# Performance work log

Measured on AMD Instinct MI355X. Metric: run time of the kernel, lower is better.

The kernel has to match this reference:

```python
import jax, jax.numpy as jnp
import numpy as np


def setup_inputs() -> dict:
    key = jax.random.key(0)
    k1, k2, k3 = jax.random.split(key, 3)
    B, S_TOT, HD = 2, 4096, 1024
    return {
        "q": jax.random.normal(k1, (B, S_TOT, HD), dtype=jnp.float32),
        "k": jax.random.normal(k2, (B, S_TOT, HD), dtype=jnp.float32),
        "v": jax.random.normal(k3, (B, S_TOT, HD), dtype=jnp.float32),
        "num_heads": 16,
        "num_shots": 4,
        "per_g": 64,
    }


def reference(q, k, v, num_heads, num_shots, per_g):
    # Equal-length shots: shot_latent_indices = [0, L, 2L, ..., s_tot] per batch.
    b, s_tot, hd = q.shape
    d = hd // num_heads
    L = s_tot // num_shots  # local shot length
    scale = 1.0 / jnp.sqrt(jnp.asarray(d, q.dtype))

    # [b, S, L, H, D]
    qs = q.reshape(b, num_shots, L, num_heads, d)
    ks = k.reshape(b, num_shots, L, num_heads, d)
    vs = v.reshape(b, num_shots, L, num_heads, d)

    # Global pool: first per_g tokens of each shot ('firstk'), shared by all shots.
    kg = ks[:, :, :per_g].reshape(b, num_shots * per_g, num_heads, d)  # [b, G, H, D]
    vg = vs[:, :, :per_g].reshape(b, num_shots * per_g, num_heads, d)

    # Block-local scores [b,S,H,L,L] and shared-global scores [b,S,H,L,G]
    s_loc = jnp.einsum("bsqhd,bskhd->bshqk", qs, ks) * scale
    s_glb = jnp.einsum("bsqhd,bghd->bshqg", qs, kg) * scale
    logits = jnp.concatenate([s_loc, s_glb], axis=-1)  # [b,S,H,L,L+G]
    p = jax.nn.softmax(logits, axis=-1)

    o_loc = jnp.einsum("bshqk,bskhd->bsqhd", p[..., :L], vs)
    o_glb = jnp.einsum("bshqg,bghd->bsqhd", p[..., L:], vg)
    out = (o_loc + o_glb).reshape(b, s_tot, hd)
    return out
```

## Files before the change

### kernel.cpp

```cpp
#include <hip/hip_runtime.h>
#include <hip/hip_bf16.h>

#define S_TOT 4096
#define HDIM  1024
#define NH    16
#define DH    64
#define L_    1024
#define NT    19

using bf16x8 = __attribute__((ext_vector_type(8))) short;
using f32x16 = __attribute__((ext_vector_type(16))) float;
using i32x4  = __attribute__((ext_vector_type(4))) int;

typedef const __attribute__((address_space(1))) unsigned int* gp1_t;
typedef __attribute__((address_space(3))) unsigned int* lp3_t;

__device__ __forceinline__ short f2bf(float f) {
    union { float f; unsigned u; } x; x.f = f;
    unsigned r = x.u + 0x7FFFu + ((x.u >> 16) & 1u);
    return (short)(r >> 16);
}

__device__ __forceinline__ unsigned cvt_pk_bf16(float lo, float hi) {
    unsigned r;
    asm("v_cvt_pk_bf16_f32 %0, %1, %2" : "=v"(r) : "v"(lo), "v"(hi));
    return r;
}

__device__ __forceinline__ float exp2_fast(float x) {
#if __has_builtin(__builtin_amdgcn_exp2f)
    return __builtin_amdgcn_exp2f(x);
#else
    return exp2f(x);
#endif
}

__device__ __forceinline__ void gload16(const void* g, void* l) {
    __builtin_amdgcn_global_load_lds((gp1_t)g, (lp3_t)(unsigned long)(l), 16, 0, 0);
}

__global__ __launch_bounds__(256) void prep_kv(
    const float* __restrict__ kf, const float* __restrict__ vf,
    short* __restrict__ kb, short* __restrict__ vb)
{
    __shared__ short st[64 * 70];
    const int bid = blockIdx.x, tid = threadIdx.x;
    if (bid < 1024) {
        const int gid = bid * 256 + tid;
        #pragma unroll
        for (int it = 0; it < 2; ++it) {
            size_t e = ((size_t)gid + (size_t)it * 262144) * 16;
            #pragma unroll
            for (int half = 0; half < 2; ++half) {
                float4 a = *(const float4*)(kf + e + half * 8);
                float4 c = *(const float4*)(kf + e + half * 8 + 4);
                bf16x8 r;
                r[0]=f2bf(a.x); r[1]=f2bf(a.y); r[2]=f2bf(a.z); r[3]=f2bf(a.w);
                r[4]=f2bf(c.x); r[5]=f2bf(c.y); r[6]=f2bf(c.z); r[7]=f2bf(c.w);
                *(bf16x8*)(kb + e + half * 8) = r;
            }
        }
    } else {
        const int vbid = bid - 1024;
        const int stile = vbid & 63, ht = (vbid >> 6) & 15, b = vbid >> 10;
        const int rt = tid >> 2, q4 = tid & 3;
        const float* src = vf + ((size_t)(b * S_TOT + stile * 64 + rt)) * HDIM + ht * 64 + q4 * 16;
        short* dst = st + rt * 70 + q4 * 16;
        #pragma unroll
        for (int i = 0; i < 4; ++i) {
            float4 x = *(const float4*)(src + i * 4);
            dst[i*4+0] = f2bf(x.x); dst[i*4+1] = f2bf(x.y);
            dst[i*4+2] = f2bf(x.z); dst[i*4+3] = f2bf(x.w);
        }
        __syncthreads();
        const int orow = tid >> 2, oq = tid & 3;
        bf16x8 o0, o1;
        #pragma unroll
        for (int j = 0; j < 8; ++j) o0[j] = st[(oq * 16 + j) * 70 + orow];
        #pragma unroll
        for (int j = 0; j < 8; ++j) o1[j] = st[(oq * 16 + 8 + j) * 70 + orow];
        short* dst2 = vb + ((size_t)((b * NH + ht) * 64 + orow)) * S_TOT + stile * 64 + oq * 16;
        *(bf16x8*)dst2 = o0;
        *(bf16x8*)(dst2 + 8) = o1;
    }
}

__global__ __launch_bounds__(128, 2) void attn_kernel(
    const float* __restrict__ qf, const short* __restrict__ kb,
    const short* __restrict__ vb, float* __restrict__ out)
{
    __shared__ __align__(16) char smem[32768];
    const int tid  = threadIdx.x;
    const int wave = tid >> 6, lane = tid & 63;
    const int hi   = lane >> 5, q32 = lane & 31;

    const int bidhw = blockIdx.x;
    const int bid = ((bidhw & 7) << 7) | (bidhw >> 3);
    const int qt = bid & 7, h = (bid >> 3) & 15, s = (bid >> 7) & 3, b = bid >> 9;

    const float CSC = 0.125f * 1.4426950408889634f;
    bf16x8 qv[2][4];
    #pragma unroll
    for (int qs = 0; qs < 2; ++qs) {
        const float* qp = qf + ((size_t)(b*S_TOT + s*L_ + qt*128 + wave*64 + qs*32 + q32)) * HDIM
                             + h * DH + hi * 8;
        #pragma unroll
        for (int d = 0; d < 4; ++d) {
            float4 x0 = *(const float4*)(qp + d * 16);
            float4 x1 = *(const float4*)(qp + d * 16 + 4);
            i32x4 u;
            u[0] = (int)cvt_pk_bf16(x0.x * CSC, x0.y * CSC);
            u[1] = (int)cvt_pk_bf16(x0.z * CSC, x0.w * CSC);
            u[2] = (int)cvt_pk_bf16(x1.x * CSC, x1.y * CSC);
            u[3] = (int)cvt_pk_bf16(x1.z * CSC, x1.w * CSC);
            qv[qs][d] = __builtin_bit_cast(bf16x8, u);
        }
    }

    const int r_low = (wave << 3) | (lane >> 3);
    const int lch   = (lane & 7) ^ (lane >> 3);
    const int krow_low = (r_low & 3) | ((r_low & 4) << 1) | ((r_low & 8) >> 1);
    const size_t ko = (size_t)krow_low * 2048 + (lch << 4);
    const size_t vo = (size_t)r_low * 8192 + (lch << 4);
    const char* kbase = (const char*)kb + ((size_t)b * S_TOT) * 2048 + h * 128;
    const char* vbase = (const char*)vb + ((size_t)(b * NH + h)) * (64ull * 8192);

    auto abs_tile_of = [&](int t) -> int {
        if (t < 16) return s * 16 + t;
        int g = t - 16; if (g >= s) ++g;
        return g * 16;
    };
    auto stage = [&](int t, int bo) {
        const int at = abs_tile_of(t);
        const char* kp = kbase + (size_t)at * 131072;
        const char* vp = vbase + (size_t)at * 128;
        char* dK = smem + bo + wave * 1024;
        char* dV = dK + 8192;
        #pragma unroll
        for (int i = 0; i < 4; ++i)
            gload16(kp + ko + (size_t)i * 32768, dK + i * 2048);
        #pragma unroll
        for (int i = 0; i < 4; ++i)
            gload16(vp + vo + (size_t)i * 131072, dV + i * 2048);
    };

    int qc[4];
    #pragma unroll
    for (int i = 0; i < 4; ++i)
        qc[i] = q32 * 128 + (((i * 2 + hi) ^ (q32 & 7)) << 4);

    f32x16 zro;
    #pragma unroll
    for (int r = 0; r < 16; ++r) zro[r] = 0.f;
    f32x16 acc[2][2];
    acc[0][0] = zro; acc[0][1] = zro; acc[1][0] = zro; acc[1][1] = zro;
    float ps[2] = {0.f, 0.f};

    #define CHUNK(RB, HF, BIAS) do {                                               \
        f32x16 S_[2];                                                              \
        {                                                                          \
            __builtin_amdgcn_s_setprio(1);                                         \
            bf16x8 f0 = *(const bf16x8*)(smem + (RB) + (HF)*4096 + qc[0]);         \
            bf16x8 f1 = *(const bf16x8*)(smem + (RB) + (HF)*4096 + qc[1]);         \
            bf16x8 f2 = *(const bf16x8*)(smem + (RB) + (HF)*4096 + qc[2]);         \
            bf16x8 f3 = *(const bf16x8*)(smem + (RB) + (HF)*4096 + qc[3]);         \
            _Pragma("unroll")                                                      \
            for (int qs = 0; qs < 2; ++qs) {                                       \
                f32x16 a = __builtin_amdgcn_mfma_f32_32x32x16_bf16(f0, qv[qs][0], zro, 0,0,0); \
                a = __builtin_amdgcn_mfma_f32_32x32x16_bf16(f1, qv[qs][1], a, 0,0,0); \
                a = __builtin_amdgcn_mfma_f32_32x32x16_bf16(f2, qv[qs][2], a, 0,0,0); \
                a = __builtin_amdgcn_mfma_f32_32x32x16_bf16(f3, qv[qs][3], a, 0,0,0); \
                S_[qs] = a;                                                        \
            }                                                                      \
            __builtin_amdgcn_s_setprio(0);                                         \
        }                                                                          \
        _Pragma("unroll")                                                          \
        for (int qs = 0; qs < 2; ++qs) {                                           \
            _Pragma("unroll")                                                      \
            for (int r = 0; r < 16; ++r)                                           \
                S_[qs][r] = exp2_fast(S_[qs][r] + (BIAS));                         \
            float s0 = (S_[qs][0] + S_[qs][1]) + (S_[qs][2] + S_[qs][3]);          \
            float s1 = (S_[qs][4] + S_[qs][5]) + (S_[qs][6] + S_[qs][7]);          \
            float s2 = (S_[qs][8] + S_[qs][9]) + (S_[qs][10] + S_[qs][11]);        \
            float s3 = (S_[qs][12] + S_[qs][13]) + (S_[qs][14] + S_[qs][15]);      \
            ps[qs] += (s0 + s1) + (s2 + s3);                                       \
        }                                                                          \
        bf16x8 pf0_[2], pf1_[2];                                                   \
        _Pragma("unroll")                                                          \
        for (int qs = 0; qs < 2; ++qs) {                                           \
            i32x4 u;                                                               \
            u[0] = (int)cvt_pk_bf16(S_[qs][0],  S_[qs][1]);                        \
            u[1] = (int)cvt_pk_bf16(S_[qs][2],  S_[qs][3]);                        \
            u[2] = (int)cvt_pk_bf16(S_[qs][4],  S_[qs][5]);                        \
            u[3] = (int)cvt_pk_bf16(S_[qs][6],  S_[qs][7]);                        \
            pf0_[qs] = __builtin_bit_cast(bf16x8, u);                              \
            u[0] = (int)cvt_pk_bf16(S_[qs][8],  S_[qs][9]);                        \
            u[1] = (int)cvt_pk_bf16(S_[qs][10], S_[qs][11]);                       \
            u[2] = (int)cvt_pk_bf16(S_[qs][12], S_[qs][13]);                       \
            u[3] = (int)cvt_pk_bf16(S_[qs][14], S_[qs][15]);                       \
            pf1_[qs] = __builtin_bit_cast(bf16x8, u);                              \
        }                                                                          \
        {                                                                          \
            __builtin_amdgcn_s_setprio(1);                                         \
            bf16x8 w00 = *(const bf16x8*)(smem + (RB) + 8192  + qc[2*(HF)]);       \
            bf16x8 w01 = *(const bf16x8*)(smem + (RB) + 8192  + qc[2*(HF)+1]);     \
            bf16x8 w10 = *(const bf16x8*)(smem + (RB) + 12288 + qc[2*(HF)]);       \
            bf16x8 w11 = *(const bf16x8*)(smem + (RB) + 12288 + qc[2*(HF)+1]);     \
            _Pragma("unroll")                                                      \
            for (int qs = 0; qs < 2; ++qs) {                                       \
                acc[qs][0] = __builtin_amdgcn_mfma_f32_32x32x16_bf16(w00, pf0_[qs], acc[qs][0], 0,0,0); \
                acc[qs][0] = __builtin_amdgcn_mfma_f32_32x32x16_bf16(w01, pf1_[qs], acc[qs][0], 0,0,0); \
                acc[qs][1] = __builtin_amdgcn_mfma_f32_32x32x16_bf16(w10, pf0_[qs], acc[qs][1], 0,0,0); \
                acc[qs][1] = __builtin_amdgcn_mfma_f32_32x32x16_bf16(w11, pf1_[qs], acc[qs][1], 0,0,0); \
            }                                                                      \
            __builtin_amdgcn_s_setprio(0);                                         \
        }                                                                          \
    } while (0)

    #define BARRIER() do {                                                         \
        __builtin_amdgcn_sched_barrier(0);                                         \
        __builtin_amdgcn_s_barrier();                                              \
        __builtin_amdgcn_sched_barrier(0);                                         \
    } while (0)

    stage(0, 0);
    asm volatile("s_waitcnt vmcnt(0)" ::: "memory");
    BARRIER();

    int bufo = 0;
    for (int t = 0; t < NT; ++t) {
        if (t + 1 < NT) {
            stage(t + 1, bufo ^ 16384);
            asm volatile("s_waitcnt vmcnt(8)" ::: "memory");
        } else {
            asm volatile("s_waitcnt vmcnt(0)" ::: "memory");
        }
        BARRIER();
        const float bias = (t == 0) ? 1.0f : 0.0f;
        CHUNK(bufo, 0, bias);
        CHUNK(bufo, 1, bias);
        BARRIER();
        bufo ^= 16384;
    }

    #pragma unroll
    for (int qs = 0; qs < 2; ++qs) {
        float tot = ps[qs] + __shfl_xor(ps[qs], 32);
        float inv = 1.0f / tot;
        const size_t orow = (size_t)(b*S_TOT + s*L_ + qt*128 + wave*64 + qs*32 + q32);
        float* op = out + orow * HDIM + h * DH;
        #pragma unroll
        for (int m = 0; m < 4; ++m) {
            float4 w0, w1;
            w0.x = acc[qs][0][4*m+0]*inv; w0.y = acc[qs][0][4*m+1]*inv;
            w0.z = acc[qs][0][4*m+2]*inv; w0.w = acc[qs][0][4*m+3]*inv;
            *(float4*)(op + 8*m + 4*hi) = w0;
            w1.x = acc[qs][1][4*m+0]*inv; w1.y = acc[qs][1][4*m+1]*inv;
            w1.z = acc[qs][1][4*m+2]*inv; w1.w = acc[qs][1][4*m+3]*inv;
            *(float4*)(op + 32 + 8*m + 4*hi) = w1;
        }
    }
}

extern "C" void kernel_launch(void* const* d_in, const int* in_sizes, int n_in,
                              void* d_out, int out_size, void* d_ws, size_t ws_size,
                              hipStream_t stream) {
    const float* q = (const float*)d_in[0];
    const float* k = (const float*)d_in[1];
    const float* v = (const float*)d_in[2];
    char* ws = (char*)d_ws;
    short* kbuf = (short*)(ws);
    short* vbuf = (short*)(ws + (16u << 20));
    prep_kv<<<dim3(3072), dim3(256), 0, stream>>>(k, v, kbuf, vbuf);
    attn_kernel<<<dim3(1024), dim3(128), 0, stream>>>(q, kbuf, vbuf, (float*)d_out);
}
```

Measured before the change: 76.05 us.

## Split KV tiles across two wave groups per block with LDS reduction

```diff
diff --git a/kernel.cpp b/kernel.cpp
--- a/kernel.cpp
+++ b/kernel.cpp
@@ -85,24 +85,26 @@
     }
 }
 
-__global__ __launch_bounds__(128, 2) void attn_kernel(
+__global__ __launch_bounds__(512, 2) void attn_kernel(
     const float* __restrict__ qf, const short* __restrict__ kb,
     const short* __restrict__ vb, float* __restrict__ out)
 {
-    __shared__ __align__(16) char smem[32768];
+    __shared__ __align__(16) char smem[67584];
     const int tid  = threadIdx.x;
     const int wave = tid >> 6, lane = tid & 63;
     const int hi   = lane >> 5, q32 = lane & 31;
+    const int khalf = wave >> 2;
+    const int qu    = wave & 3;
 
     const int bidhw = blockIdx.x;
-    const int bid = ((bidhw & 7) << 7) | (bidhw >> 3);
-    const int qt = bid & 7, h = (bid >> 3) & 15, s = (bid >> 7) & 3, b = bid >> 9;
+    const int bid = ((bidhw & 7) << 6) | (bidhw >> 3);
+    const int qt = bid & 3, h = (bid >> 2) & 15, s = (bid >> 6) & 3, b = bid >> 8;
 
     const float CSC = 0.125f * 1.4426950408889634f;
     bf16x8 qv[2][4];
     #pragma unroll
     for (int qs = 0; qs < 2; ++qs) {
-        const float* qp = qf + ((size_t)(b*S_TOT + s*L_ + qt*128 + wave*64 + qs*32 + q32)) * HDIM
+        const float* qp = qf + ((size_t)(b*S_TOT + s*L_ + qt*256 + qu*64 + qs*32 + q32)) * HDIM
                              + h * DH + hi * 8;
         #pragma unroll
         for (int d = 0; d < 4; ++d) {
@@ -117,11 +119,12 @@
         }
     }
 
-    const int r_low = (wave << 3) | (lane >> 3);
-    const int lch   = (lane & 7) ^ (lane >> 3);
-    const int krow_low = (r_low & 3) | ((r_low & 4) << 1) | ((r_low & 8) >> 1);
-    const size_t ko = (size_t)krow_low * 2048 + (lch << 4);
-    const size_t vo = (size_t)r_low * 8192 + (lch << 4);
+    const int sid  = (qu << 6) | lane;
+    const int srow = sid >> 3;
+    const int slch = (sid & 7) ^ (srow & 7);
+    const int skrow = (srow & 0x33) | ((srow & 4) << 1) | ((srow & 8) >> 1);
+    const size_t ko = (size_t)skrow * 2048 + (slch << 4);
+    const size_t vo = (size_t)srow  * 8192 + (slch << 4);
     const char* kbase = (const char*)kb + ((size_t)b * S_TOT) * 2048 + h * 128;
     const char* vbase = (const char*)vb + ((size_t)(b * NH + h)) * (64ull * 8192);
 
@@ -130,18 +133,16 @@
         int g = t - 16; if (g >= s) ++g;
         return g * 16;
     };
-    auto stage = [&](int t, int bo) {
-        const int at = abs_tile_of(t);
+    auto stageT = [&](int tile, int bufbase) {
+        const int at = abs_tile_of(tile);
         const char* kp = kbase + (size_t)at * 131072;
         const char* vp = vbase + (size_t)at * 128;
-        char* dK = smem + bo + wave * 1024;
+        char* dK = smem + bufbase + khalf * 16384 + (qu << 10);
         char* dV = dK + 8192;
-        #pragma unroll
-        for (int i = 0; i < 4; ++i)
-            gload16(kp + ko + (size_t)i * 32768, dK + i * 2048);
-        #pragma unroll
-        for (int i = 0; i < 4; ++i)
-            gload16(vp + vo + (size_t)i * 131072, dV + i * 2048);
+        gload16(kp + ko,          dK);
+        gload16(kp + ko + 65536,  dK + 4096);
+        gload16(vp + vo,          dV);
+        gload16(vp + vo + 262144, dV + 4096);
     };
 
     int qc[4];
@@ -156,7 +157,7 @@
     acc[0][0] = zro; acc[0][1] = zro; acc[1][0] = zro; acc[1][1] = zro;
     float ps[2] = {0.f, 0.f};
 
-    #define CHUNK(RB, HF, BIAS) do {                                               \
+    #define CHUNK(RB, HF, BIASOP) do {                                             \
         f32x16 S_[2];                                                              \
         {                                                                          \
             __builtin_amdgcn_s_setprio(1);                                         \
@@ -177,13 +178,10 @@
         _Pragma("unroll")                                                          \
         for (int qs = 0; qs < 2; ++qs) {                                           \
             _Pragma("unroll")                                                      \
-            for (int r = 0; r < 16; ++r)                                           \
-                S_[qs][r] = exp2_fast(S_[qs][r] + (BIAS));                         \
-            float s0 = (S_[qs][0] + S_[qs][1]) + (S_[qs][2] + S_[qs][3]);          \
-            float s1 = (S_[qs][4] + S_[qs][5]) + (S_[qs][6] + S_[qs][7]);          \
-            float s2 = (S_[qs][8] + S_[qs][9]) + (S_[qs][10] + S_[qs][11]);        \
-            float s3 = (S_[qs][12] + S_[qs][13]) + (S_[qs][14] + S_[qs][15]);      \
-            ps[qs] += (s0 + s1) + (s2 + s3);                                       \
+            for (int r = 0; r < 16; ++r) {                                         \
+                float p = exp2_fast(S_[qs][r] BIASOP);                             \
+                S_[qs][r] = p; ps[qs] += p;                                        \
+            }                                                                      \
         }                                                                          \
         bf16x8 pf0_[2], pf1_[2];                                                   \
         _Pragma("unroll")                                                          \
@@ -217,47 +215,79 @@
         }                                                                          \
     } while (0)
 
-    #define BARRIER() do {                                                         \
-        __builtin_amdgcn_sched_barrier(0);                                         \
-        __builtin_amdgcn_s_barrier();                                              \
-        __builtin_amdgcn_sched_barrier(0);                                         \
-    } while (0)
-
-    stage(0, 0);
-    asm volatile("s_waitcnt vmcnt(0)" ::: "memory");
-    BARRIER();
-
-    int bufo = 0;
-    for (int t = 0; t < NT; ++t) {
-        if (t + 1 < NT) {
-            stage(t + 1, bufo ^ 16384);
-            asm volatile("s_waitcnt vmcnt(8)" ::: "memory");
-        } else {
-            asm volatile("s_waitcnt vmcnt(0)" ::: "memory");
-        }
-        BARRIER();
-        const float bias = (t == 0) ? 1.0f : 0.0f;
-        CHUNK(bufo, 0, bias);
-        CHUNK(bufo, 1, bias);
-        BARRIER();
-        bufo ^= 16384;
-    }
-
-    #pragma unroll
-    for (int qs = 0; qs < 2; ++qs) {
-        float tot = ps[qs] + __shfl_xor(ps[qs], 32);
-        float inv = 1.0f / tot;
-        const size_t orow = (size_t)(b*S_TOT + s*L_ + qt*128 + wave*64 + qs*32 + q32);
-        float* op = out + orow * HDIM + h * DH;
-        #pragma unroll
-        for (int m = 0; m < 4; ++m) {
-            float4 w0, w1;
-            w0.x = acc[qs][0][4*m+0]*inv; w0.y = acc[qs][0][4*m+1]*inv;
-            w0.z = acc[qs][0][4*m+2]*inv; w0.w = acc[qs][0][4*m+3]*inv;
-            *(float4*)(op + 8*m + 4*hi) = w0;
-            w1.x = acc[qs][1][4*m+0]*inv; w1.y = acc[qs][1][4*m+1]*inv;
-            w1.z = acc[qs][1][4*m+2]*inv; w1.w = acc[qs][1][4*m+3]*inv;
-            *(float4*)(op + 32 + 8*m + 4*hi) = w1;
+    stageT(khalf ? 10 : 0, 0);
+
+    for (int t = 0; t < 10; ++t) {
+        asm volatile("s_waitcnt vmcnt(0)" ::: "memory");
+        __builtin_amdgcn_sched_barrier(0);
+        __builtin_amdgcn_s_barrier();
+        __builtin_amdgcn_sched_barrier(0);
+
+        const int cb = (t & 1) << 15;
+        if (khalf == 0) { if (t < 9) stageT(t + 1,  cb ^ 32768); }
+        else            { if (t < 8) stageT(11 + t, cb ^ 32768); }
+
+        const int rb = cb + khalf * 16384;
+        if (t == 0) {
+            if (khalf == 0) { CHUNK(rb, 0, +1.0f); CHUNK(rb, 1, +1.0f); }
+            else            { CHUNK(rb, 0, );      CHUNK(rb, 1, );      }
+        } else if (khalf == 0 || t < 9) {
+            CHUNK(rb, 0, ); CHUNK(rb, 1, );
+        }
+    }
+
+    ps[0] += __shfl_xor(ps[0], 32);
+    ps[1] += __shfl_xor(ps[1], 32);
+
+    if (khalf == 0) {
+        char* mb = smem + (qu << 14);
+        #pragma unroll
+        for (int qs = 0; qs < 2; ++qs)
+            #pragma unroll
+            for (int dh = 0; dh < 2; ++dh)
+                #pragma unroll
+                for (int m = 0; m < 4; ++m) {
+                    float4 w;
+                    w.x = acc[qs][dh][4*m+0]; w.y = acc[qs][dh][4*m+1];
+                    w.z = acc[qs][dh][4*m+2]; w.w = acc[qs][dh][4*m+3];
+                    *(float4*)(mb + ((((qs*2+dh)*4 + m)) << 10) + (lane << 4)) = w;
+                }
+        *(float2*)(smem + 65536 + (qu << 9) + (lane << 3)) = make_float2(ps[0], ps[1]);
+        asm volatile("s_waitcnt lgkmcnt(0)" ::: "memory");
+    }
+    __builtin_amdgcn_sched_barrier(0);
+    __builtin_amdgcn_s_barrier();
+    __builtin_amdgcn_sched_barrier(0);
+
+    if (khalf == 1) {
+        char* mb = smem + (qu << 14);
+        #pragma unroll
+        for (int qs = 0; qs < 2; ++qs)
+            #pragma unroll
+            for (int dh = 0; dh < 2; ++dh)
+                #pragma unroll
+                for (int m = 0; m < 4; ++m) {
+                    float4 w = *(const float4*)(mb + ((((qs*2+dh)*4 + m)) << 10) + (lane << 4));
+                    acc[qs][dh][4*m+0] += w.x; acc[qs][dh][4*m+1] += w.y;
+                    acc[qs][dh][4*m+2] += w.z; acc[qs][dh][4*m+3] += w.w;
+                }
+        float2 pp = *(const float2*)(smem + 65536 + (qu << 9) + (lane << 3));
+        float tot[2] = {ps[0] + pp.x, ps[1] + pp.y};
+        #pragma unroll
+        for (int qs = 0; qs < 2; ++qs) {
+            float inv = 1.0f / tot[qs];
+            const size_t orow = (size_t)(b*S_TOT + s*L_ + qt*256 + qu*64 + qs*32 + q32);
+            float* op = out + orow * HDIM + h * DH;
+            #pragma unroll
+            for (int m = 0; m < 4; ++m) {
+                float4 w0, w1;
+                w0.x = acc[qs][0][4*m+0]*inv; w0.y = acc[qs][0][4*m+1]*inv;
+                w0.z = acc[qs][0][4*m+2]*inv; w0.w = acc[qs][0][4*m+3]*inv;
+                *(float4*)(op + 8*m + 4*hi) = w0;
+                w1.x = acc[qs][1][4*m+0]*inv; w1.y = acc[qs][1][4*m+1]*inv;
+                w1.z = acc[qs][1][4*m+2]*inv; w1.w = acc[qs][1][4*m+3]*inv;
+                *(float4*)(op + 32 + 8*m + 4*hi) = w1;
+            }
         }
     }
 }
@@ -272,5 +302,5 @@
     short* kbuf = (short*)(ws);
     short* vbuf = (short*)(ws + (16u << 20));
     prep_kv<<<dim3(3072), dim3(256), 0, stream>>>(k, v, kbuf, vbuf);
-    attn_kernel<<<dim3(1024), dim3(128), 0, stream>>>(q, kbuf, vbuf, (float*)d_out);
-}
+    attn_kernel<<<dim3(512), dim3(512), 0, stream>>>(q, kbuf, vbuf, (float*)d_out);
+}
```

Result: slower. 79.56 us (+4.6%).
